# Performance work log

Hardware: AMD Instinct MI355X
Metric: run time of the kernel (lower is better)

The kernel has to match this reference:

```python
import jax, jax.numpy as jnp
import numpy as np

# Sizes: N nodes, E directed edges, C input channels, H hidden channels.
N = 50000
E = 800000
C = 64
H = 64
EPS = 1e-5


def _bn(h, gamma, beta):
    # LazyBatchNorm: per-channel normalization over all rows (batch stats).
    m = h.mean(axis=0)
    v = ((h - m) ** 2).mean(axis=0)
    return (h - m) * jax.lax.rsqrt(v + EPS) * gamma + beta


def setup_inputs() -> dict:
    key = jax.random.key(0)
    ks = jax.random.split(key, 8)

    def glorot(k, shape):
        return jax.random.normal(k, shape, dtype=jnp.float32) / jnp.sqrt(jnp.float32(shape[0]))

    x = jax.random.normal(ks[0], (N, C), dtype=jnp.float32)
    edge_index = jax.random.randint(ks[1], (2, E), 0, N)
    return {
        "x": x,
        "edge_index": edge_index,
        "W_unite": glorot(ks[2], (2 * C, H)),
        "b_unite": jnp.zeros((H,), jnp.float32),
        "g1": jnp.ones((H,), jnp.float32),
        "be1": jnp.zeros((H,), jnp.float32),
        "W_gconv": glorot(ks[3], (2 * H, H)),
        "b_gconv": jnp.zeros((H,), jnp.float32),
        "g2": jnp.ones((H,), jnp.float32),
        "be2": jnp.zeros((H,), jnp.float32),
        "W_transfer": glorot(ks[4], (2 * H, H)),
        "b_transfer": jnp.zeros((H,), jnp.float32),
        "W_lin": glorot(ks[5], (H, H)),
        "b_lin": jnp.zeros((H,), jnp.float32),
        "g3": jnp.ones((H,), jnp.float32),
        "be3": jnp.zeros((H,), jnp.float32),
    }


def reference(x, edge_index, W_unite, b_unite, g1, be1, W_gconv, b_gconv, g2, be2,
              W_transfer, b_transfer, W_lin, b_lin, g3, be3):
    n = x.shape[0]
    src_e = edge_index[0]
    dst_e = edge_index[1]
    # linmaps1: ptensors0 -> ptensors1 with singleton reference domains (identity on data).
    # unite1: each node's domain becomes {node} U N(node). Row layout: first n rows
    # are self rows (atom i in domain i), then E rows (atom src in domain dst).
    self_idx = jnp.arange(n)
    rows_src = jnp.concatenate([self_idx, src_e])   # atom index per row
    rows_dom = jnp.concatenate([self_idx, dst_e])   # domain owner per row

    # --- unite1 (2 linmaps: gather + broadcast-of-domain-sum), then linear + BN + relu
    f = x[rows_src]                                           # [R, C] gather
    dsum = jax.ops.segment_sum(f, rows_dom, num_segments=n)   # [N, C]
    h = jnp.concatenate([f, dsum[rows_dom]], axis=-1) @ W_unite + b_unite  # [R, H]
    h = jax.nn.relu(_bn(h, g1, be1))
    # dropout1: identity in eval mode

    # --- higher graph conv: reduce each domain to order-0, aggregate over edges,
    # broadcast back and combine with local rows (2 maps), linear + BN + relu
    s = jax.ops.segment_sum(h, rows_dom, num_segments=n)          # [N, H] per-domain reduce
    msg = jax.ops.segment_sum(s[src_e], dst_e, num_segments=n)    # [N, H] neighborhood sum
    h2 = jnp.concatenate([h, msg[rows_dom]], axis=-1) @ W_gconv + b_gconv  # [R, H]
    h2 = jax.nn.relu(_bn(h2, g2, be2))
    # dropout2: identity

    # --- transfer back to ptensors0 (singleton domains): per-atom reduce over all rows
    # referencing that atom + the atom's own self row (2 maps), linear + BN + relu.
    # NOTE: the source reuses batchnorm2 here (it is assigned twice in __init__).
    agg = jax.ops.segment_sum(h2, rows_src, num_segments=n)       # [N, H]
    t = jnp.concatenate([h2[:n], agg], axis=-1) @ W_transfer + b_transfer  # [N, H]
    t = jax.nn.relu(_bn(t, g2, be2))
    # dropout3: identity

    # --- final linear + relu, BN + relu
    out = jax.nn.relu(t @ W_lin + b_lin)
    out = jax.nn.relu(_bn(out, g3, be3))
    # dropout4: identity
    return out
```

## Files before the change

kernel.cpp:

```cpp
#include <hip/hip_runtime.h>
#include <cstdint>
#include <math.h>

#define NN 50000
#define EE 800000
#define RR 850000
#define NT_N 3125
#define NT_R 53125
#define NBLK_H2 2048
#define NBLK_MM 512
#define CHUNK 512
#define NCH 98

typedef short  bf16x8 __attribute__((ext_vector_type(8)));
typedef float  f32x4  __attribute__((ext_vector_type(4)));

__device__ __forceinline__ float bf2f(unsigned short b) {
    unsigned int u = ((unsigned int)b) << 16;
    return __builtin_bit_cast(float, u);
}
__device__ __forceinline__ unsigned short f2bf(float f) {
    unsigned int u = __builtin_bit_cast(unsigned int, f);
    u = u + 0x7fffu + ((u >> 16) & 1u);
    return (unsigned short)(u >> 16);
}
__device__ __forceinline__ void atomAddD(double* p, double v) { unsafeAtomicAdd(p, v); }
__device__ __forceinline__ int atomAddI(int* p, int v) { return atomicAdd(p, v); }

__device__ __forceinline__ void split8(const float* p, bf16x8& hi, bf16x8& lo) {
    f32x4 v0 = *reinterpret_cast<const f32x4*>(p);
    f32x4 v1 = *reinterpret_cast<const f32x4*>(p + 4);
#pragma unroll
    for (int j = 0; j < 4; j++) {
        unsigned short h0 = f2bf(v0[j]);
        hi[j] = (short)h0; lo[j] = (short)f2bf(v0[j] - bf2f(h0));
        unsigned short h1 = f2bf(v1[j]);
        hi[4 + j] = (short)h1; lo[4 + j] = (short)f2bf(v1[j] - bf2f(h1));
    }
}
__device__ __forceinline__ void split8r(const float* v, bf16x8& hi, bf16x8& lo) {
#pragma unroll
    for (int j = 0; j < 8; j++) {
        unsigned short h = f2bf(v[j]);
        hi[j] = (short)h; lo[j] = (short)f2bf(v[j] - bf2f(h));
    }
}

template <bool RELU, bool STATS>
__device__ __forceinline__ void epi_tile(float* wl, int lane, const f32x4* acc,
                                         const float* bv, float* __restrict__ gout,
                                         int tile, double* ssum, double* ssq) {
    const int m = lane & 15, quad = lane >> 4;
#pragma unroll
    for (int ct = 0; ct < 4; ct++)
#pragma unroll
        for (int i = 0; i < 4; i++) {
            float val = acc[ct][i] + bv[ct];
            if (RELU) val = fmaxf(val, 0.f);
            wl[(quad * 4 + i) * 68 + ct * 16 + m] = val;
            if (STATS) { ssum[ct] += (double)val; ssq[ct] += (double)val * (double)val; }
        }
    asm volatile("s_waitcnt lgkmcnt(0)" ::: "memory");
#pragma unroll
    for (int j = 0; j < 4; j++) {
        int row = j * 4 + quad;
        f32x4 vv = *reinterpret_cast<const f32x4*>(wl + row * 68 + m * 4);
        *reinterpret_cast<f32x4*>(gout + ((size_t)(tile << 4) + row) * 64 + m * 4) = vv;
    }
}

__device__ __forceinline__ void stats_block_out(float* ldsbase, int lane, int wid,
                                                const double* ssum, const double* ssq,
                                                double* __restrict__ part) {
    const int m = lane & 15, quad = lane >> 4;
    double* dl = (double*)ldsbase;
    __syncthreads();
#pragma unroll
    for (int ct = 0; ct < 4; ct++) {
        double sv = ssum[ct], qv = ssq[ct];
        sv += __shfl_xor(sv, 16, 64); sv += __shfl_xor(sv, 32, 64);
        qv += __shfl_xor(qv, 16, 64); qv += __shfl_xor(qv, 32, 64);
        if (quad == 0) {
            dl[wid * 128 + ct * 16 + m]      = sv;
            dl[wid * 128 + 64 + ct * 16 + m] = qv;
        }
    }
    __syncthreads();
    int tid = wid * 64 + lane;
    if (tid < 128) {
        double tot = dl[tid] + dl[128 + tid] + dl[256 + tid] + dl[384 + tid];
        part[(size_t)blockIdx.x * 128 + tid] = tot;
    }
}

__global__ void k_red(const double* __restrict__ p, int nblk, double* __restrict__ raw) {
    int t = threadIdx.x;
    double acc = 0.0;
    for (int b = blockIdx.x; b < nblk; b += gridDim.x)
        acc += p[(size_t)b * 128 + t];
    atomAddD(&raw[t], acc);
}

__global__ void k_deg(const int* __restrict__ ei, int* __restrict__ od, int* __restrict__ id) {
    int e = blockIdx.x * 256 + threadIdx.x;
    atomAddI(&od[ei[e]], 1);
    atomAddI(&id[ei[EE + e]], 1);
}

__global__ void k_scanA(const int* __restrict__ id, const int* __restrict__ od,
                        int* __restrict__ csum) {
    int arr = blockIdx.x / NCH;
    int ch  = blockIdx.x % NCH;
    const int* cnt = arr ? od : id;
    int t = threadIdx.x;
    int i0 = ch * CHUNK + t;
    int s = 0;
    if (i0 < NN) s += cnt[i0];
    if (i0 + 256 < NN && (t + 256) < CHUNK) s += cnt[i0 + 256];
#pragma unroll
    for (int d = 1; d < 64; d <<= 1) s += __shfl_xor(s, d, 64);
    __shared__ int ws[4];
    if ((t & 63) == 0) ws[t >> 6] = s;
    __syncthreads();
    if (t == 0) csum[arr * NCH + ch] = ws[0] + ws[1] + ws[2] + ws[3];
}

__global__ void k_scanB(int* __restrict__ csum) {
    __shared__ int part[256];
    int t = threadIdx.x;
    int arr = t >> 7, slot = t & 127;
    int v = (slot < NCH) ? csum[arr * NCH + slot] : 0;
    part[t] = v;
    __syncthreads();
#pragma unroll
    for (int d = 1; d < 128; d <<= 1) {
        int val = (slot >= d) ? part[t - d] : 0;
        __syncthreads();
        part[t] += val;
        __syncthreads();
    }
    if (slot < NCH)
        csum[arr * NCH + slot] = (slot == 0) ? 0 : part[t - 1];
}

__global__ void k_scanC(const int* __restrict__ id, const int* __restrict__ od,
                        const int* __restrict__ csum,
                        int* __restrict__ off, int* __restrict__ cursor,
                        int* __restrict__ off_s, int* __restrict__ cursor_s) {
    int arr = blockIdx.x / NCH;
    int ch  = blockIdx.x % NCH;
    const int* cnt = arr ? od : id;
    int* o  = arr ? off_s : off;
    int* cu = arr ? cursor_s : cursor;
    int t = threadIdx.x;
    int idx = ch * CHUNK + 2 * t;
    int e0 = 0, e1 = 0;
    if (idx < NN)     e0 = cnt[idx];
    if (idx + 1 < NN) e1 = cnt[idx + 1];
    int p = e0 + e1;
    int lane = t & 63;
    int incl = p;
#pragma unroll
    for (int d = 1; d < 64; d <<= 1) {
        int v = __shfl_up(incl, d, 64);
        if (lane >= d) incl += v;
    }
    __shared__ int wsum[4];
    if (lane == 63) wsum[t >> 6] = incl;
    __syncthreads();
    int w = t >> 6;
    int wbase = 0;
#pragma unroll
    for (int i = 0; i < 4; i++) if (i < w) wbase += wsum[i];
    int base = csum[arr * NCH + ch] + wbase + (incl - p);
    if (idx < NN)     { o[idx]     = base;      cu[idx]     = base; }
    if (idx + 1 < NN) { o[idx + 1] = base + e0; cu[idx + 1] = base + e0; }
    if (blockIdx.x == 0 && t == 0) { off[NN] = EE; off_s[NN] = EE; }
}

__global__ void k_fill(const int* __restrict__ ei, int* __restrict__ cursor,
                       unsigned int* __restrict__ sd_s) {
    int e = blockIdx.x * 256 + threadIdx.x;
    int s = ei[e], d = ei[EE + e];
    int p = atomAddI(&cursor[d], 1);
    sd_s[p] = (unsigned int)s | ((unsigned int)d << 16);
}

__global__ void k_fill2(const unsigned int* __restrict__ sd_s, int* __restrict__ cursor_s,
                        int* __restrict__ perm_s) {
    int p = blockIdx.x * 256 + threadIdx.x;
    int s = (int)(sd_s[p] & 0xFFFFu);
    int q = atomAddI(&cursor_s[s], 1);
    perm_s[q] = p;
}

__global__ void k_dsum_csr(const float* __restrict__ x, const int* __restrict__ off,
                           const unsigned int* __restrict__ sd_s, float* __restrict__ dsum) {
    int team = (blockIdx.x * 256 + threadIdx.x) >> 6;
    int c = threadIdx.x & 63;
    float a[16];
#pragma unroll
    for (int j = 0; j < 16; j++) a[j] = 0.f;
    a[0] = x[(size_t)team * 64 + c];
    int e = off[team], e1 = off[team + 1];
    for (; e + 15 < e1; e += 16)
#pragma unroll
        for (int j = 0; j < 16; j++) a[j] += x[(size_t)(sd_s[e + j] & 0xFFFFu) * 64 + c];
    for (; e + 3 < e1; e += 4)
#pragma unroll
        for (int j = 0; j < 4; j++) a[j] += x[(size_t)(sd_s[e + j] & 0xFFFFu) * 64 + c];
    for (; e < e1; e++) a[0] += x[(size_t)(sd_s[e] & 0xFFFFu) * 64 + c];
#pragma unroll
    for (int j = 0; j < 8; j++) a[j] += a[j + 8];
#pragma unroll
    for (int j = 0; j < 4; j++) a[j] += a[j + 4];
    dsum[(size_t)team * 64 + c] = (a[0] + a[1]) + (a[2] + a[3]);
}

__global__ void k_uv3(const float* __restrict__ x, const float* __restrict__ dsum,
                      const float* __restrict__ W, float* __restrict__ u,
                      float* __restrict__ v, float* __restrict__ u2) {
    __shared__ float lds[4][16 * 68];
    const int lane = threadIdx.x & 63;
    const int wid = threadIdx.x >> 6;
    const int m = lane & 15, quad = lane >> 4;
    const int gwave = (blockIdx.x * blockDim.x + threadIdx.x) >> 6;
    const int nwaves = (gridDim.x * blockDim.x) >> 6;
    float* wl = lds[wid];

    bf16x8 wfh[4][4], wfl[4][4];
#pragma unroll
    for (int kk = 0; kk < 4; kk++)
#pragma unroll
        for (int ct = 0; ct < 4; ct++) {
            float wv[8];
#pragma unroll
            for (int j = 0; j < 8; j++)
                wv[j] = W[(kk * 32 + quad * 8 + j) * 64 + ct * 16 + m];
            split8r(wv, wfh[kk][ct], wfl[kk][ct]);
        }
    float zb[4] = {0.f, 0.f, 0.f, 0.f};

    for (int tile = gwave; tile < NT_N; tile += nwaves) {
        const int r = (tile << 4) + m;
        bf16x8 ah[4], al[4];
        split8(x    + (size_t)r * 64 + quad * 8,      ah[0], al[0]);
        split8(x    + (size_t)r * 64 + 32 + quad * 8, ah[1], al[1]);
        split8(dsum + (size_t)r * 64 + quad * 8,      ah[2], al[2]);
        split8(dsum + (size_t)r * 64 + 32 + quad * 8, ah[3], al[3]);

        f32x4 zero = {0.f, 0.f, 0.f, 0.f};
        f32x4 aU[4], aV[4], aU2[4];
#pragma unroll
        for (int ct = 0; ct < 4; ct++) {
            aU[ct] = zero; aV[ct] = zero; aU2[ct] = zero;
#pragma unroll
            for (int kk = 0; kk < 2; kk++) {
                aU[ct]  = __builtin_amdgcn_mfma_f32_16x16x32_bf16(al[kk],   wfh[kk][ct],   aU[ct],  0, 0, 0);
                aU[ct]  = __builtin_amdgcn_mfma_f32_16x16x32_bf16(ah[kk],   wfl[kk][ct],   aU[ct],  0, 0, 0);
                aU[ct]  = __builtin_amdgcn_mfma_f32_16x16x32_bf16(ah[kk],   wfh[kk][ct],   aU[ct],  0, 0, 0);
                aV[ct]  = __builtin_amdgcn_mfma_f32_16x16x32_bf16(al[kk+2], wfh[kk+2][ct], aV[ct],  0, 0, 0);
                aV[ct]  = __builtin_amdgcn_mfma_f32_16x16x32_bf16(ah[kk+2], wfl[kk+2][ct], aV[ct],  0, 0, 0);
                aV[ct]  = __builtin_amdgcn_mfma_f32_16x16x32_bf16(ah[kk+2], wfh[kk+2][ct], aV[ct],  0, 0, 0);
                aU2[ct] = __builtin_amdgcn_mfma_f32_16x16x32_bf16(al[kk+2], wfh[kk][ct],   aU2[ct], 0, 0, 0);
                aU2[ct] = __builtin_amdgcn_mfma_f32_16x16x32_bf16(ah[kk+2], wfl[kk][ct],   aU2[ct], 0, 0, 0);
                aU2[ct] = __builtin_amdgcn_mfma_f32_16x16x32_bf16(ah[kk+2], wfh[kk][ct],   aU2[ct], 0, 0, 0);
            }
        }
        epi_tile<false, false>(wl, lane, aU,  zb, u,  tile, nullptr, nullptr);
        epi_tile<false, false>(wl, lane, aV,  zb, v,  tile, nullptr, nullptr);
        epi_tile<false, false>(wl, lane, aU2, zb, u2, tile, nullptr, nullptr);
    }
}

__global__ void k_stats1a(const float* __restrict__ u, const float* __restrict__ v,
                          const float* __restrict__ u2, const int* __restrict__ od,
                          const int* __restrict__ id, double* __restrict__ stats_raw) {
    __shared__ double lsum[4][64], lsq[4][64];
    int tid = threadIdx.x, c = tid & 63, w = tid >> 6;
    double a1 = 0.0, a2 = 0.0;
    for (int n = blockIdx.x * 4 + w; n < NN; n += gridDim.x * 4) {
        double uu = u[(size_t)n * 64 + c], vv = v[(size_t)n * 64 + c];
        double uu2 = u2[(size_t)n * 64 + c];
        double wod = 1.0 + od[n], wid = 1.0 + id[n];
        a1 += wod * uu + wid * vv;
        a2 += wod * uu * uu + wid * vv * vv + 2.0 * vv * uu2;
    }
    lsum[w][c] = a1; lsq[w][c] = a2;
    __syncthreads();
    if (w == 0) {
        a1 = lsum[0][c] + lsum[1][c] + lsum[2][c] + lsum[3][c];
        a2 = lsq[0][c] + lsq[1][c] + lsq[2][c] + lsq[3][c];
        atomAddD(&stats_raw[c], a1);
        atomAddD(&stats_raw[64 + c], a2);
    }
}

__global__ void k_fin1(const double* __restrict__ raw, const float* __restrict__ b,
                       float* __restrict__ fin, double inv_cnt) {
    int c = threadIdx.x;
    double m1 = raw[c] * inv_cnt;
    double var = raw[64 + c] * inv_cnt - m1 * m1;
    if (var < 0.0) var = 0.0;
    fin[c] = (float)(m1 + (double)b[c]);
    fin[64 + c] = (float)(1.0 / sqrt(var + 1e-5));
}

__global__ void k_fin(const double* __restrict__ raw, float* __restrict__ fin, double inv_cnt) {
    int c = threadIdx.x;
    double mean = raw[c] * inv_cnt;
    double var = raw[64 + c] * inv_cnt - mean * mean;
    if (var < 0.0) var = 0.0;
    fin[c] = (float)mean;
    fin[64 + c] = (float)(1.0 / sqrt(var + 1e-5));
}

__global__ void k_s1h(const float* __restrict__ u, const float* __restrict__ v,
                      const int* __restrict__ off, const unsigned int* __restrict__ sd_s,
                      const float* __restrict__ b_un, const float* __restrict__ fin,
                      const float* __restrict__ g1, const float* __restrict__ be1,
                      float* __restrict__ s_tab, unsigned short* __restrict__ hb) {
    int team = (blockIdx.x * 256 + threadIdx.x) >> 6;
    int c = threadIdx.x & 63;
    float sc = fin[64 + c] * g1[c];
    float tsh = (b_un[c] - fin[c]) * sc + be1[c];
    float vn = v[(size_t)team * 64 + c];
    float a[16];
#pragma unroll
    for (int j = 0; j < 16; j++) a[j] = 0.f;
    float hs = fmaxf((u[(size_t)team * 64 + c] + vn) * sc + tsh, 0.f);
    a[0] = hs;
    hb[(size_t)team * 64 + c] = f2bf(hs);
    int e = off[team], e1 = off[team + 1];
    for (; e + 15 < e1; e += 16)
#pragma unroll
        for (int j = 0; j < 16; j++) {
            float h = fmaxf((u[(size_t)(sd_s[e + j] & 0xFFFFu) * 64 + c] + vn) * sc + tsh, 0.f);
            a[j] += h;
            hb[(size_t)(NN + e + j) * 64 + c] = f2bf(h);
        }
    for (; e + 3 < e1; e += 4)
#pragma unroll
        for (int j = 0; j < 4; j++) {
            float h = fmaxf((u[(size_t)(sd_s[e + j] & 0xFFFFu) * 64 + c] + vn) * sc + tsh, 0.f);
            a[j] += h;
            hb[(size_t)(NN + e + j) * 64 + c] = f2bf(h);
        }
    for (; e < e1; e++) {
        float h = fmaxf((u[(size_t)(sd_s[e] & 0xFFFFu) * 64 + c] + vn) * sc + tsh, 0.f);
        a[0] += h;
        hb[(size_t)(NN + e) * 64 + c] = f2bf(h);
    }
#pragma unroll
    for (int j = 0; j < 8; j++) a[j] += a[j + 8];
#pragma unroll
    for (int j = 0; j < 4; j++) a[j] += a[j + 4];
    s_tab[(size_t)team * 64 + c] = (a[0] + a[1]) + (a[2] + a[3]);
}

__global__ void k_msg_csr(const int* __restrict__ off, const unsigned int* __restrict__ sd_s,
                          const float* __restrict__ s_tab, float* __restrict__ msg) {
    int team = (blockIdx.x * 256 + threadIdx.x) >> 6;
    int c = threadIdx.x & 63;
    float a[16];
#pragma unroll
    for (int j = 0; j < 16; j++) a[j] = 0.f;
    int e = off[team], e1 = off[team + 1];
    for (; e + 15 < e1; e += 16)
#pragma unroll
        for (int j = 0; j < 16; j++) a[j] += s_tab[(size_t)(sd_s[e + j] & 0xFFFFu) * 64 + c];
    for (; e + 3 < e1; e += 4)
#pragma unroll
        for (int j = 0; j < 4; j++) a[j] += s_tab[(size_t)(sd_s[e + j] & 0xFFFFu) * 64 + c];
    for (; e < e1; e++) a[0] += s_tab[(size_t)(sd_s[e] & 0xFFFFu) * 64 + c];
#pragma unroll
    for (int j = 0; j < 8; j++) a[j] += a[j + 8];
#pragma unroll
    for (int j = 0; j < 4; j++) a[j] += a[j + 4];
    msg[(size_t)team * 64 + c] = (a[0] + a[1]) + (a[2] + a[3]);
}

__global__ void k_mb(const float* __restrict__ in, float* __restrict__ outp,
                     const float* __restrict__ W) {
    __shared__ float lds[4][16 * 68];
    const int lane = threadIdx.x & 63;
    const int wid = threadIdx.x >> 6;
    const int m = lane & 15, quad = lane >> 4;
    const int gwave = (blockIdx.x * blockDim.x + threadIdx.x) >> 6;
    const int nwaves = (gridDim.x * blockDim.x) >> 6;
    float* wl = lds[wid];

    bf16x8 wfh[2][4], wfl[2][4];
#pragma unroll
    for (int kk = 0; kk < 2; kk++)
#pragma unroll
        for (int ct = 0; ct < 4; ct++) {
            float wv[8];
#pragma unroll
            for (int j = 0; j < 8; j++)
                wv[j] = W[(kk * 32 + quad * 8 + j) * 64 + ct * 16 + m];
            split8r(wv, wfh[kk][ct], wfl[kk][ct]);
        }
    float zb[4] = {0.f, 0.f, 0.f, 0.f};

    for (int tile = gwave; tile < NT_N; tile += nwaves) {
        const int r = (tile << 4) + m;
        bf16x8 ah[2], al[2];
        split8(in + (size_t)r * 64 + quad * 8,      ah[0], al[0]);
        split8(in + (size_t)r * 64 + 32 + quad * 8, ah[1], al[1]);

        f32x4 zero = {0.f, 0.f, 0.f, 0.f};
        f32x4 acc[4];
#pragma unroll
        for (int ct = 0; ct < 4; ct++) {
            acc[ct] = zero;
#pragma unroll
            for (int kk = 0; kk < 2; kk++) {
                acc[ct] = __builtin_amdgcn_mfma_f32_16x16x32_bf16(al[kk], wfh[kk][ct], acc[ct], 0, 0, 0);
                acc[ct] = __builtin_amdgcn_mfma_f32_16x16x32_bf16(ah[kk], wfl[kk][ct], acc[ct], 0, 0, 0);
                acc[ct] = __builtin_amdgcn_mfma_f32_16x16x32_bf16(ah[kk], wfh[kk][ct], acc[ct], 0, 0, 0);
            }
        }
        epi_tile<false, false>(wl, lane, acc, zb, outp, tile, nullptr, nullptr);
    }
}

__global__ void k_h2(const unsigned short* __restrict__ hb, unsigned short* __restrict__ h2b,
                     const float* __restrict__ mb, const unsigned int* __restrict__ sd_s,
                     const float* __restrict__ W, const float* __restrict__ b_gc,
                     double* __restrict__ part) {
    __shared__ float lds[4][16 * 68];
    const int lane = threadIdx.x & 63;
    const int wid = threadIdx.x >> 6;
    const int m = lane & 15, quad = lane >> 4;
    const int gwave = (blockIdx.x * blockDim.x + threadIdx.x) >> 6;
    const int nwaves = (gridDim.x * blockDim.x) >> 6;
    float* wl = lds[wid];

    bf16x8 wfh[2][4], wfl[2][4];
#pragma unroll
    for (int kk = 0; kk < 2; kk++)
#pragma unroll
        for (int ct = 0; ct < 4; ct++) {
            float wv[8];
#pragma unroll
            for (int j = 0; j < 8; j++)
                wv[j] = W[(kk * 32 + quad * 8 + j) * 64 + ct * 16 + m];
            split8r(wv, wfh[kk][ct], wfl[kk][ct]);
        }

    float bv[4];
#pragma unroll
    for (int ct = 0; ct < 4; ct++) bv[ct] = b_gc[ct * 16 + m];

    double ssum[4] = {0,0,0,0}, ssq[4] = {0,0,0,0};

    for (int tile = gwave; tile < NT_R; tile += nwaves) {
        const int r = (tile << 4) + m;
        int dm = (tile < NT_N) ? r : (int)(sd_s[r - NN] >> 16);

        bf16x8 ah[2];
        ah[0] = *reinterpret_cast<const bf16x8*>(hb + (size_t)r * 64 + quad * 8);
        ah[1] = *reinterpret_cast<const bf16x8*>(hb + (size_t)r * 64 + 32 + quad * 8);

        f32x4 zero = {0.f, 0.f, 0.f, 0.f};
        f32x4 acc[4];
#pragma unroll
        for (int ct = 0; ct < 4; ct++) {
            acc[ct] = zero;
#pragma unroll
            for (int kk = 0; kk < 2; kk++) {
                acc[ct] = __builtin_amdgcn_mfma_f32_16x16x32_bf16(ah[kk], wfl[kk][ct], acc[ct], 0, 0, 0);
                acc[ct] = __builtin_amdgcn_mfma_f32_16x16x32_bf16(ah[kk], wfh[kk][ct], acc[ct], 0, 0, 0);
            }
        }

#pragma unroll
        for (int i = 0; i < 4; i++) {
            int dmv = __shfl(dm, (lane & 48) + quad * 4 + i, 64);
#pragma unroll
            for (int ct = 0; ct < 4; ct++) {
                float val = acc[ct][i] + bv[ct] + mb[(size_t)dmv * 64 + ct * 16 + m];
                wl[(quad * 4 + i) * 68 + ct * 16 + m] = val;
                ssum[ct] += (double)val;
                ssq[ct]  += (double)val * (double)val;
            }
        }
        asm volatile("s_waitcnt lgkmcnt(0)" ::: "memory");
#pragma unroll
        for (int j = 0; j < 4; j++) {
            int row = j * 4 + quad;
            f32x4 vv = *reinterpret_cast<const f32x4*>(wl + row * 68 + m * 4);
            unsigned int p0 = (unsigned int)f2bf(vv[0]) | ((unsigned int)f2bf(vv[1]) << 16);
            unsigned int p1 = (unsigned int)f2bf(vv[2]) | ((unsigned int)f2bf(vv[3]) << 16);
            uint2 pk; pk.x = p0; pk.y = p1;
            *reinterpret_cast<uint2*>(h2b + ((size_t)(tile << 4) + row) * 64 + m * 4) = pk;
        }
    }

    stats_block_out(&lds[0][0], lane, wid, ssum, ssq, part);
}

__global__ void k_agg_csr(const unsigned short* __restrict__ h2b, const int* __restrict__ off_s,
                          const int* __restrict__ perm_s, const float* __restrict__ fin2,
                          const float* __restrict__ g2, const float* __restrict__ be2,
                          float* __restrict__ agg) {
    int n = (blockIdx.x * 256 + threadIdx.x) >> 6;
    int c = threadIdx.x & 63;
    float sc = fin2[64 + c] * g2[c];
    float sh = be2[c] - fin2[c] * sc;
    float a[16];
#pragma unroll
    for (int j = 0; j < 16; j++) a[j] = 0.f;
    a[0] = fmaxf(bf2f(h2b[(size_t)n * 64 + c]) * sc + sh, 0.f);
    int q = off_s[n], q1 = off_s[n + 1];
    for (; q + 15 < q1; q += 16)
#pragma unroll
        for (int j = 0; j < 16; j++) {
            float hv = bf2f(h2b[(size_t)(NN + perm_s[q + j]) * 64 + c]);
            a[j] += fmaxf(hv * sc + sh, 0.f);
        }
    for (; q + 3 < q1; q += 4)
#pragma unroll
        for (int j = 0; j < 4; j++) {
            float hv = bf2f(h2b[(size_t)(NN + perm_s[q + j]) * 64 + c]);
            a[j] += fmaxf(hv * sc + sh, 0.f);
        }
    for (; q < q1; q++) {
        float hv = bf2f(h2b[(size_t)(NN + perm_s[q]) * 64 + c]);
        a[0] += fmaxf(hv * sc + sh, 0.f);
    }
#pragma unroll
    for (int j = 0; j < 8; j++) a[j] += a[j + 8];
#pragma unroll
    for (int j = 0; j < 4; j++) a[j] += a[j + 4];
    agg[(size_t)n * 64 + c] = (a[0] + a[1]) + (a[2] + a[3]);
}

__global__ void k_mm3(const unsigned short* __restrict__ h2b, const float* __restrict__ agg,
                      const float* __restrict__ W, const float* __restrict__ bias,
                      const float* __restrict__ fin2, const float* __restrict__ g2,
                      const float* __restrict__ be2,
                      float* __restrict__ outp, double* __restrict__ part) {
    __shared__ float lds[4][16 * 68];
    const int lane = threadIdx.x & 63;
    const int wid = threadIdx.x >> 6;
    const int m = lane & 15, quad = lane >> 4;
    const int gwave = (blockIdx.x * blockDim.x + threadIdx.x) >> 6;
    const int nwaves = (gridDim.x * blockDim.x) >> 6;
    float* wl = lds[wid];

    bf16x8 wfh[4][4], wfl[4][4];
#pragma unroll
    for (int kk = 0; kk < 4; kk++)
#pragma unroll
        for (int ct = 0; ct < 4; ct++) {
            float wv[8];
#pragma unroll
            for (int j = 0; j < 8; j++)
                wv[j] = W[(kk * 32 + quad * 8 + j) * 64 + ct * 16 + m];
            split8r(wv, wfh[kk][ct], wfl[kk][ct]);
        }

    float bv[4];
#pragma unroll
    for (int ct = 0; ct < 4; ct++) bv[ct] = bias[ct * 16 + m];

    float s2f[2][8], t2f[2][8];
#pragma unroll
    for (int kk = 0; kk < 2; kk++)
#pragma unroll
        for (int j = 0; j < 8; j++) {
            int c = kk * 32 + quad * 8 + j;
            float sc = fin2[64 + c] * g2[c];
            s2f[kk][j] = sc;
            t2f[kk][j] = be2[c] - fin2[c] * sc;
        }

    double ssum[4] = {0,0,0,0}, ssq[4] = {0,0,0,0};

    for (int tile = gwave; tile < NT_N; tile += nwaves) {
        const int r = (tile << 4) + m;
        bf16x8 ah[4], al[4];
#pragma unroll
        for (int kk = 0; kk < 2; kk++) {
            bf16x8 hv = *reinterpret_cast<const bf16x8*>(h2b + (size_t)r * 64 + kk * 32 + quad * 8);
            float tv[8];
#pragma unroll
            for (int j = 0; j < 8; j++) {
                float f = bf2f((unsigned short)hv[j]);
                tv[j] = fmaxf(f * s2f[kk][j] + t2f[kk][j], 0.f);
            }
            split8r(tv, ah[kk], al[kk]);
        }
        split8(agg + (size_t)r * 64 + quad * 8,      ah[2], al[2]);
        split8(agg + (size_t)r * 64 + 32 + quad * 8, ah[3], al[3]);

        f32x4 zero = {0.f, 0.f, 0.f, 0.f};
        f32x4 acc[4];
#pragma unroll
        for (int ct = 0; ct < 4; ct++) {
            acc[ct] = zero;
#pragma unroll
            for (int kk = 0; kk < 4; kk++)
                acc[ct] = __builtin_amdgcn_mfma_f32_16x16x32_bf16(al[kk], wfh[kk][ct], acc[ct], 0, 0, 0);
#pragma unroll
            for (int kk = 0; kk < 4; kk++)
                acc[ct] = __builtin_amdgcn_mfma_f32_16x16x32_bf16(ah[kk], wfl[kk][ct], acc[ct], 0, 0, 0);
#pragma unroll
            for (int kk = 0; kk < 4; kk++)
                acc[ct] = __builtin_amdgcn_mfma_f32_16x16x32_bf16(ah[kk], wfh[kk][ct], acc[ct], 0, 0, 0);
        }

        epi_tile<false, true>(wl, lane, acc, bv, outp, tile, ssum, ssq);
    }

    stats_block_out(&lds[0][0], lane, wid, ssum, ssq, part);
}

__global__ void k_mm4(const float* __restrict__ tpre, const float* __restrict__ W,
                      const float* __restrict__ bias, const float* __restrict__ fin3,
                      const float* __restrict__ g2, const float* __restrict__ be2,
                      float* __restrict__ outp, double* __restrict__ part) {
    __shared__ float lds[4][16 * 68];
    const int lane = threadIdx.x & 63;
    const int wid = threadIdx.x >> 6;
    const int m = lane & 15, quad = lane >> 4;
    const int gwave = (blockIdx.x * blockDim.x + threadIdx.x) >> 6;
    const int nwaves = (gridDim.x * blockDim.x) >> 6;
    float* wl = lds[wid];

    bf16x8 wfh[2][4], wfl[2][4];
#pragma unroll
    for (int kk = 0; kk < 2; kk++)
#pragma unroll
        for (int ct = 0; ct < 4; ct++) {
            float wv[8];
#pragma unroll
            for (int j = 0; j < 8; j++)
                wv[j] = W[(kk * 32 + quad * 8 + j) * 64 + ct * 16 + m];
            split8r(wv, wfh[kk][ct], wfl[kk][ct]);
        }

    float bv[4];
#pragma unroll
    for (int ct = 0; ct < 4; ct++) bv[ct] = bias[ct * 16 + m];

    float sc[2][8], sh[2][8];
#pragma unroll
    for (int kk = 0; kk < 2; kk++)
#pragma unroll
        for (int j = 0; j < 8; j++) {
            int c = kk * 32 + quad * 8 + j;
            float s = fin3[64 + c] * g2[c];
            sc[kk][j] = s;
            sh[kk][j] = be2[c] - fin3[c] * s;
        }

    double ssum[4] = {0,0,0,0}, ssq[4] = {0,0,0,0};

    for (int tile = gwave; tile < NT_N; tile += nwaves) {
        const int r = (tile << 4) + m;
        bf16x8 ah[2], al[2];
#pragma unroll
        for (int kk = 0; kk < 2; kk++) {
            f32x4 v0 = *reinterpret_cast<const f32x4*>(tpre + (size_t)r * 64 + kk * 32 + quad * 8);
            f32x4 v1 = *reinterpret_cast<const f32x4*>(tpre + (size_t)r * 64 + kk * 32 + quad * 8 + 4);
            float tv[8];
#pragma unroll
            for (int j = 0; j < 4; j++) {
                tv[j]     = fmaxf(v0[j] * sc[kk][j]     + sh[kk][j],     0.f);
                tv[4 + j] = fmaxf(v1[j] * sc[kk][4 + j] + sh[kk][4 + j], 0.f);
            }
            split8r(tv, ah[kk], al[kk]);
        }

        f32x4 zero = {0.f, 0.f, 0.f, 0.f};
        f32x4 acc[4];
#pragma unroll
        for (int ct = 0; ct < 4; ct++) {
            acc[ct] = zero;
#pragma unroll
            for (int kk = 0; kk < 2; kk++) {
                acc[ct] = __builtin_amdgcn_mfma_f32_16x16x32_bf16(al[kk], wfh[kk][ct], acc[ct], 0, 0, 0);
                acc[ct] = __builtin_amdgcn_mfma_f32_16x16x32_bf16(ah[kk], wfl[kk][ct], acc[ct], 0, 0, 0);
                acc[ct] = __builtin_amdgcn_mfma_f32_16x16x32_bf16(ah[kk], wfh[kk][ct], acc[ct], 0, 0, 0);
            }
        }

        epi_tile<true, true>(wl, lane, acc, bv, outp, tile, ssum, ssq);
    }

    stats_block_out(&lds[0][0], lane, wid, ssum, ssq, part);
}

__global__ void k_out(const float* __restrict__ op, const float* __restrict__ fin,
                      const float* __restrict__ g, const float* __restrict__ be,
                      float* __restrict__ out) {
    int i = blockIdx.x * 256 + threadIdx.x;
    int c = i & 63;
    out[i] = fmaxf((op[i] - fin[c]) * fin[64 + c] * g[c] + be[c], 0.f);
}

extern "C" void kernel_launch(void* const* d_in, const int* in_sizes, int n_in,
                              void* d_out, int out_size, void* d_ws, size_t ws_size,
                              hipStream_t stream) {
    const float* x    = (const float*)d_in[0];
    const int*   ei   = (const int*)d_in[1];
    const float* W_un = (const float*)d_in[2];
    const float* b_un = (const float*)d_in[3];
    const float* g1   = (const float*)d_in[4];
    const float* be1  = (const float*)d_in[5];
    const float* W_gc = (const float*)d_in[6];
    const float* b_gc = (const float*)d_in[7];
    const float* g2   = (const float*)d_in[8];
    const float* be2  = (const float*)d_in[9];
    const float* W_tr = (const float*)d_in[10];
    const float* b_tr = (const float*)d_in[11];
    const float* W_li = (const float*)d_in[12];
    const float* b_li = (const float*)d_in[13];
    const float* g3   = (const float*)d_in[14];
    const float* be3  = (const float*)d_in[15];

    float* ws = (float*)d_ws;
    const size_t FN = (size_t)NN * 64;
    const size_t FR = (size_t)RR * 64;
    float* P0 = ws;
    float* P1 = ws + FN;
    float* P2 = ws + 2 * FN;
    float* H  = ws + 3 * FN;
    float* u      = P0;
    float* v      = P1;
    float* s_tab  = P2;
    int*   csum   = (int*)P2;
    float* dsum   = H;
    float* u2     = H + FN;
    unsigned short* hb  = (unsigned short*)H;
    unsigned short* h2b = (unsigned short*)H + FR;
    float* msg    = P0;
    float* agg    = P1;
    float* tpre   = P2;
    float* outpre = P0;
    double* part_h2 = (double*)P2;
    double* part_m3 = (double*)P0;
    double* part_m4 = (double*)P1;
    double*       stats_raw = (double*)(H + FR);
    int*          od        = (int*)(stats_raw + 512);
    int*          id        = od + NN;
    int*          off       = id + NN;
    int*          cursor    = off + NN + 1;
    int*          off_s     = cursor + NN;
    int*          cursor_s  = off_s + NN + 1;
    unsigned int* sd_s      = (unsigned int*)(cursor_s + NN);
    int*          perm_s    = (int*)(sd_s + EE);
    float*        stats_fin = (float*)(perm_s + EE);

    hipMemsetAsync(stats_raw, 0, 512 * sizeof(double) + 2 * NN * sizeof(int), stream);

    k_deg  <<<3125, 256, 0, stream>>>(ei, od, id);
    k_scanA<<<2 * NCH, 256, 0, stream>>>(id, od, csum);
    k_scanB<<<1, 256, 0, stream>>>(csum);
    k_scanC<<<2 * NCH, 256, 0, stream>>>(id, od, csum, off, cursor, off_s, cursor_s);
    k_fill <<<3125, 256, 0, stream>>>(ei, cursor, sd_s);
    k_fill2<<<3125, 256, 0, stream>>>(sd_s, cursor_s, perm_s);

    k_dsum_csr<<<12500, 256, 0, stream>>>(x, off, sd_s, dsum);
    k_uv3<<<512, 256, 0, stream>>>(x, dsum, W_un, u, v, u2);

    k_stats1a<<<256, 256, 0, stream>>>(u, v, u2, od, id, stats_raw + 0);
    k_fin1<<<1, 64, 0, stream>>>(stats_raw + 0, b_un, stats_fin + 0, 1.0 / (double)RR);
    k_s1h<<<12500, 256, 0, stream>>>(u, v, off, sd_s, b_un, stats_fin + 0, g1, be1,
                                     s_tab, hb);
    k_msg_csr<<<12500, 256, 0, stream>>>(off, sd_s, s_tab, msg);
    k_mb<<<512, 256, 0, stream>>>(msg, msg, W_gc + 64 * 64);

    k_h2<<<NBLK_H2, 256, 0, stream>>>(hb, h2b, msg, sd_s, W_gc, b_gc, part_h2);
    k_red<<<32, 128, 0, stream>>>(part_h2, NBLK_H2, stats_raw + 128);
    k_fin<<<1, 64, 0, stream>>>(stats_raw + 128, stats_fin + 128, 1.0 / (double)RR);
    k_agg_csr<<<12500, 256, 0, stream>>>(h2b, off_s, perm_s, stats_fin + 128, g2, be2, agg);

    k_mm3<<<NBLK_MM, 256, 0, stream>>>(h2b, agg, W_tr, b_tr, stats_fin + 128, g2, be2,
                                       tpre, part_m3);
    k_red<<<16, 128, 0, stream>>>(part_m3, NBLK_MM, stats_raw + 256);
    k_fin<<<1, 64, 0, stream>>>(stats_raw + 256, stats_fin + 256, 1.0 / (double)NN);

    k_mm4<<<NBLK_MM, 256, 0, stream>>>(tpre, W_li, b_li, stats_fin + 256, g2, be2,
                                       outpre, part_m4);
    k_red<<<16, 128, 0, stream>>>(part_m4, NBLK_MM, stats_raw + 384);
    k_fin<<<1, 64, 0, stream>>>(stats_raw + 384, stats_fin + 384, 1.0 / (double)NN);

    k_out<<<12500, 256, 0, stream>>>(outpre, stats_fin + 384, g3, be3, (float*)d_out);
}
```

Before: 722.6 us.

## Store gathered node tables (x, u, s) in bf16 to halve gather traffic

Adds a conversion kernel that writes x as bf16, and reads that copy in the edge-gather dsum kernel. k_uv3 now writes u in bf16 and k_s1h writes the per-domain sum table in bf16. The s1h and msg gathers read those 2-byte tables, halving bytes per random row access in the three edge-gather kernels. The cost is an extra conversion pass and bf16 rounding of features that were fp32, which may hurt accuracy, particularly in the summed s table.

Result: no change. 716.7 us (-0.8%).

```diff
diff --git a/kernel.cpp b/kernel.cpp
--- a/kernel.cpp
+++ b/kernel.cpp
@@ -69,6 +69,26 @@
     }
 }
 
+__device__ __forceinline__ void epi_tile_b16(float* wl, int lane, const f32x4* acc,
+                                             unsigned short* __restrict__ gout, int tile) {
+    const int m = lane & 15, quad = lane >> 4;
+#pragma unroll
+    for (int ct = 0; ct < 4; ct++)
+#pragma unroll
+        for (int i = 0; i < 4; i++)
+            wl[(quad * 4 + i) * 68 + ct * 16 + m] = acc[ct][i];
+    asm volatile("s_waitcnt lgkmcnt(0)" ::: "memory");
+#pragma unroll
+    for (int j = 0; j < 4; j++) {
+        int row = j * 4 + quad;
+        f32x4 vv = *reinterpret_cast<const f32x4*>(wl + row * 68 + m * 4);
+        unsigned int p0 = (unsigned int)f2bf(vv[0]) | ((unsigned int)f2bf(vv[1]) << 16);
+        unsigned int p1 = (unsigned int)f2bf(vv[2]) | ((unsigned int)f2bf(vv[3]) << 16);
+        uint2 pk; pk.x = p0; pk.y = p1;
+        *reinterpret_cast<uint2*>(gout + ((size_t)(tile << 4) + row) * 64 + m * 4) = pk;
+    }
+}
+
 __device__ __forceinline__ void stats_block_out(float* ldsbase, int lane, int wid,
                                                 const double* ssum, const double* ssq,
                                                 double* __restrict__ part) {
@@ -105,6 +125,11 @@
     int e = blockIdx.x * 256 + threadIdx.x;
     atomAddI(&od[ei[e]], 1);
     atomAddI(&id[ei[EE + e]], 1);
+}
+
+__global__ void k_xc(const float* __restrict__ x, unsigned short* __restrict__ xb) {
+    int i = blockIdx.x * 256 + threadIdx.x;
+    xb[i] = f2bf(x[i]);
 }
 
 __global__ void k_scanA(const int* __restrict__ id, const int* __restrict__ od,
@@ -194,7 +219,8 @@
     perm_s[q] = p;
 }
 
-__global__ void k_dsum_csr(const float* __restrict__ x, const int* __restrict__ off,
+__global__ void k_dsum_csr(const float* __restrict__ x, const unsigned short* __restrict__ xb,
+                           const int* __restrict__ off,
                            const unsigned int* __restrict__ sd_s, float* __restrict__ dsum) {
     int team = (blockIdx.x * 256 + threadIdx.x) >> 6;
     int c = threadIdx.x & 63;
@@ -205,11 +231,11 @@
     int e = off[team], e1 = off[team + 1];
     for (; e + 15 < e1; e += 16)
 #pragma unroll
-        for (int j = 0; j < 16; j++) a[j] += x[(size_t)(sd_s[e + j] & 0xFFFFu) * 64 + c];
+        for (int j = 0; j < 16; j++) a[j] += bf2f(xb[(size_t)(sd_s[e + j] & 0xFFFFu) * 64 + c]);
     for (; e + 3 < e1; e += 4)
 #pragma unroll
-        for (int j = 0; j < 4; j++) a[j] += x[(size_t)(sd_s[e + j] & 0xFFFFu) * 64 + c];
-    for (; e < e1; e++) a[0] += x[(size_t)(sd_s[e] & 0xFFFFu) * 64 + c];
+        for (int j = 0; j < 4; j++) a[j] += bf2f(xb[(size_t)(sd_s[e + j] & 0xFFFFu) * 64 + c]);
+    for (; e < e1; e++) a[0] += bf2f(xb[(size_t)(sd_s[e] & 0xFFFFu) * 64 + c]);
 #pragma unroll
     for (int j = 0; j < 8; j++) a[j] += a[j + 8];
 #pragma unroll
@@ -218,7 +244,7 @@
 }
 
 __global__ void k_uv3(const float* __restrict__ x, const float* __restrict__ dsum,
-                      const float* __restrict__ W, float* __restrict__ u,
+                      const float* __restrict__ W, unsigned short* __restrict__ ub,
                       float* __restrict__ v, float* __restrict__ u2) {
     __shared__ float lds[4][16 * 68];
     const int lane = threadIdx.x & 63;
@@ -267,20 +293,21 @@
                 aU2[ct] = __builtin_amdgcn_mfma_f32_16x16x32_bf16(ah[kk+2], wfh[kk][ct],   aU2[ct], 0, 0, 0);
             }
         }
-        epi_tile<false, false>(wl, lane, aU,  zb, u,  tile, nullptr, nullptr);
+        epi_tile_b16(wl, lane, aU, ub, tile);
         epi_tile<false, false>(wl, lane, aV,  zb, v,  tile, nullptr, nullptr);
         epi_tile<false, false>(wl, lane, aU2, zb, u2, tile, nullptr, nullptr);
     }
 }
 
-__global__ void k_stats1a(const float* __restrict__ u, const float* __restrict__ v,
+__global__ void k_stats1a(const unsigned short* __restrict__ ub, const float* __restrict__ v,
                           const float* __restrict__ u2, const int* __restrict__ od,
                           const int* __restrict__ id, double* __restrict__ stats_raw) {
     __shared__ double lsum[4][64], lsq[4][64];
     int tid = threadIdx.x, c = tid & 63, w = tid >> 6;
     double a1 = 0.0, a2 = 0.0;
     for (int n = blockIdx.x * 4 + w; n < NN; n += gridDim.x * 4) {
-        double uu = u[(size_t)n * 64 + c], vv = v[(size_t)n * 64 + c];
+        double uu = (double)bf2f(ub[(size_t)n * 64 + c]);
+        double vv = v[(size_t)n * 64 + c];
         double uu2 = u2[(size_t)n * 64 + c];
         double wod = 1.0 + od[n], wid = 1.0 + id[n];
         a1 += wod * uu + wid * vv;
@@ -315,11 +342,11 @@
     fin[64 + c] = (float)(1.0 / sqrt(var + 1e-5));
 }
 
-__global__ void k_s1h(const float* __restrict__ u, const float* __restrict__ v,
+__global__ void k_s1h(const unsigned short* __restrict__ ub, const float* __restrict__ v,
                       const int* __restrict__ off, const unsigned int* __restrict__ sd_s,
                       const float* __restrict__ b_un, const float* __restrict__ fin,
                       const float* __restrict__ g1, const float* __restrict__ be1,
-                      float* __restrict__ s_tab, unsigned short* __restrict__ hb) {
+                      unsigned short* __restrict__ stb, unsigned short* __restrict__ hb) {
     int team = (blockIdx.x * 256 + threadIdx.x) >> 6;
     int c = threadIdx.x & 63;
     float sc = fin[64 + c] * g1[c];
@@ -328,26 +355,26 @@
     float a[16];
 #pragma unroll
     for (int j = 0; j < 16; j++) a[j] = 0.f;
-    float hs = fmaxf((u[(size_t)team * 64 + c] + vn) * sc + tsh, 0.f);
+    float hs = fmaxf((bf2f(ub[(size_t)team * 64 + c]) + vn) * sc + tsh, 0.f);
     a[0] = hs;
     hb[(size_t)team * 64 + c] = f2bf(hs);
     int e = off[team], e1 = off[team + 1];
     for (; e + 15 < e1; e += 16)
 #pragma unroll
         for (int j = 0; j < 16; j++) {
-            float h = fmaxf((u[(size_t)(sd_s[e + j] & 0xFFFFu) * 64 + c] + vn) * sc + tsh, 0.f);
+            float h = fmaxf((bf2f(ub[(size_t)(sd_s[e + j] & 0xFFFFu) * 64 + c]) + vn) * sc + tsh, 0.f);
             a[j] += h;
             hb[(size_t)(NN + e + j) * 64 + c] = f2bf(h);
         }
     for (; e + 3 < e1; e += 4)
 #pragma unroll
         for (int j = 0; j < 4; j++) {
-            float h = fmaxf((u[(size_t)(sd_s[e + j] & 0xFFFFu) * 64 + c] + vn) * sc + tsh, 0.f);
+            float h = fmaxf((bf2f(ub[(size_t)(sd_s[e + j] & 0xFFFFu) * 64 + c]) + vn) * sc + tsh, 0.f);
             a[j] += h;
             hb[(size_t)(NN + e + j) * 64 + c] = f2bf(h);
         }
     for (; e < e1; e++) {
-        float h = fmaxf((u[(size_t)(sd_s[e] & 0xFFFFu) * 64 + c] + vn) * sc + tsh, 0.f);
+        float h = fmaxf((bf2f(ub[(size_t)(sd_s[e] & 0xFFFFu) * 64 + c]) + vn) * sc + tsh, 0.f);
         a[0] += h;
         hb[(size_t)(NN + e) * 64 + c] = f2bf(h);
     }
@@ -355,11 +382,11 @@
     for (int j = 0; j < 8; j++) a[j] += a[j + 8];
 #pragma unroll
     for (int j = 0; j < 4; j++) a[j] += a[j + 4];
-    s_tab[(size_t)team * 64 + c] = (a[0] + a[1]) + (a[2] + a[3]);
+    stb[(size_t)team * 64 + c] = f2bf((a[0] + a[1]) + (a[2] + a[3]));
 }
 
 __global__ void k_msg_csr(const int* __restrict__ off, const unsigned int* __restrict__ sd_s,
-                          const float* __restrict__ s_tab, float* __restrict__ msg) {
+                          const unsigned short* __restrict__ stb, float* __restrict__ msg) {
     int team = (blockIdx.x * 256 + threadIdx.x) >> 6;
     int c = threadIdx.x & 63;
     float a[16];
@@ -368,11 +395,11 @@
     int e = off[team], e1 = off[team + 1];
     for (; e + 15 < e1; e += 16)
 #pragma unroll
-        for (int j = 0; j < 16; j++) a[j] += s_tab[(size_t)(sd_s[e + j] & 0xFFFFu) * 64 + c];
+        for (int j = 0; j < 16; j++) a[j] += bf2f(stb[(size_t)(sd_s[e + j] & 0xFFFFu) * 64 + c]);
     for (; e + 3 < e1; e += 4)
 #pragma unroll
-        for (int j = 0; j < 4; j++) a[j] += s_tab[(size_t)(sd_s[e + j] & 0xFFFFu) * 64 + c];
-    for (; e < e1; e++) a[0] += s_tab[(size_t)(sd_s[e] & 0xFFFFu) * 64 + c];
+        for (int j = 0; j < 4; j++) a[j] += bf2f(stb[(size_t)(sd_s[e + j] & 0xFFFFu) * 64 + c]);
+    for (; e < e1; e++) a[0] += bf2f(stb[(size_t)(sd_s[e] & 0xFFFFu) * 64 + c]);
 #pragma unroll
     for (int j = 0; j < 8; j++) a[j] += a[j + 8];
 #pragma unroll
@@ -729,12 +756,13 @@
     float* P1 = ws + FN;
     float* P2 = ws + 2 * FN;
     float* H  = ws + 3 * FN;
-    float* u      = P0;
+    unsigned short* ub   = (unsigned short*)P0;
     float* v      = P1;
-    float* s_tab  = P2;
+    unsigned short* stb  = (unsigned short*)P2;
     int*   csum   = (int*)P2;
     float* dsum   = H;
     float* u2     = H + FN;
+    unsigned short* xb16 = (unsigned short*)(H + 2 * FN);
     unsigned short* hb  = (unsigned short*)H;
     unsigned short* h2b = (unsigned short*)H + FR;
     float* msg    = P0;
@@ -758,20 +786,21 @@
     hipMemsetAsync(stats_raw, 0, 512 * sizeof(double) + 2 * NN * sizeof(int), stream);
 
     k_deg  <<<3125, 256, 0, stream>>>(ei, od, id);
+    k_xc   <<<12500, 256, 0, stream>>>(x, xb16);
     k_scanA<<<2 * NCH, 256, 0, stream>>>(id, od, csum);
     k_scanB<<<1, 256, 0, stream>>>(csum);
     k_scanC<<<2 * NCH, 256, 0, stream>>>(id, od, csum, off, cursor, off_s, cursor_s);
     k_fill <<<3125, 256, 0, stream>>>(ei, cursor, sd_s);
     k_fill2<<<3125, 256, 0, stream>>>(sd_s, cursor_s, perm_s);
 
-    k_dsum_csr<<<12500, 256, 0, stream>>>(x, off, sd_s, dsum);
-    k_uv3<<<512, 256, 0, stream>>>(x, dsum, W_un, u, v, u2);
-
-    k_stats1a<<<256, 256, 0, stream>>>(u, v, u2, od, id, stats_raw + 0);
+    k_dsum_csr<<<12500, 256, 0, stream>>>(x, xb16, off, sd_s, dsum);
+    k_uv3<<<512, 256, 0, stream>>>(x, dsum, W_un, ub, v, u2);
+
+    k_stats1a<<<256, 256, 0, stream>>>(ub, v, u2, od, id, stats_raw + 0);
     k_fin1<<<1, 64, 0, stream>>>(stats_raw + 0, b_un, stats_fin + 0, 1.0 / (double)RR);
-    k_s1h<<<12500, 256, 0, stream>>>(u, v, off, sd_s, b_un, stats_fin + 0, g1, be1,
-                                     s_tab, hb);
-    k_msg_csr<<<12500, 256, 0, stream>>>(off, sd_s, s_tab, msg);
+    k_s1h<<<12500, 256, 0, stream>>>(ub, v, off, sd_s, b_un, stats_fin + 0, g1, be1,
+                                     stb, hb);
+    k_msg_csr<<<12500, 256, 0, stream>>>(off, sd_s, stb, msg);
     k_mb<<<512, 256, 0, stream>>>(msg, msg, W_gc + 64 * 64);
 
     k_h2<<<NBLK_H2, 256, 0, stream>>>(hb, h2b, msg, sd_s, W_gc, b_gc, part_h2);
```
